# Performance work log

Measured on AMD Instinct MI355X. Metric: run time of the kernel, lower is better.

## Reference

```python
import jax, jax.numpy as jnp
import numpy as np

H = 512   # hidden_size
IN = 5    # input_size
OUT = 2   # output_size
B = 2048
T_HIST = 50


def _lstm_cell(x, h, c, W_ih, W_hh, b_ih, b_hh):
    # PyTorch gate order: i, f, g, o
    z = x @ W_ih.T + h @ W_hh.T + (b_ih + b_hh)
    i, f, g, o = jnp.split(z, 4, axis=-1)
    i = jax.nn.sigmoid(i)
    f = jax.nn.sigmoid(f)
    g = jnp.tanh(g)
    o = jax.nn.sigmoid(o)
    c2 = f * c + i * g
    h2 = o * jnp.tanh(c2)
    return h2, c2


def setup_inputs() -> dict:
    key = jax.random.key(0)
    ks = jax.random.split(key, 20)
    s = 0.05
    inp = {
        "history": jax.random.normal(ks[0], (B, T_HIST, IN), dtype=jnp.float32),
        "future_frames": 30,
        # encoder layer 0 (input IN) and layer 1 (input H)
        "enc_W_ih0": jax.random.normal(ks[1], (4 * H, IN)) * s,
        "enc_W_hh0": jax.random.normal(ks[2], (4 * H, H)) * s,
        "enc_b_ih0": jnp.zeros((4 * H,), jnp.float32),
        "enc_b_hh0": jnp.zeros((4 * H,), jnp.float32),
        "enc_W_ih1": jax.random.normal(ks[3], (4 * H, H)) * s,
        "enc_W_hh1": jax.random.normal(ks[4], (4 * H, H)) * s,
        "enc_b_ih1": jnp.zeros((4 * H,), jnp.float32),
        "enc_b_hh1": jnp.zeros((4 * H,), jnp.float32),
        # decoder layer 0 (input OUT) and layer 1 (input H)
        "dec_W_ih0": jax.random.normal(ks[5], (4 * H, OUT)) * s,
        "dec_W_hh0": jax.random.normal(ks[6], (4 * H, H)) * s,
        "dec_b_ih0": jnp.zeros((4 * H,), jnp.float32),
        "dec_b_hh0": jnp.zeros((4 * H,), jnp.float32),
        "dec_W_ih1": jax.random.normal(ks[7], (4 * H, H)) * s,
        "dec_W_hh1": jax.random.normal(ks[8], (4 * H, H)) * s,
        "dec_b_ih1": jnp.zeros((4 * H,), jnp.float32),
        "dec_b_hh1": jnp.zeros((4 * H,), jnp.float32),
        # output head
        "out_W": jax.random.normal(ks[9], (OUT, H)) * s,
        "out_b": jnp.zeros((OUT,), jnp.float32),
    }
    return inp


def reference(history, enc_W_ih0, enc_W_hh0, enc_b_ih0, enc_b_hh0,
              enc_W_ih1, enc_W_hh1, enc_b_ih1, enc_b_hh1,
              dec_W_ih0, dec_W_hh0, dec_b_ih0, dec_b_hh0,
              dec_W_ih1, dec_W_hh1, dec_b_ih1, dec_b_hh1,
              out_W, out_b, future_frames):
    batch = history.shape[0]
    z = jnp.zeros((batch, H), history.dtype)

    # ----- encoder: 2-layer LSTM over history, scan over time -----
    def enc_step(carry, x_t):
        h0, c0, h1, c1 = carry
        h0, c0 = _lstm_cell(x_t, h0, c0, enc_W_ih0, enc_W_hh0, enc_b_ih0, enc_b_hh0)
        h1, c1 = _lstm_cell(h0, h1, c1, enc_W_ih1, enc_W_hh1, enc_b_ih1, enc_b_hh1)
        return (h0, c0, h1, c1), None

    xs = jnp.swapaxes(history, 0, 1)  # [T, B, IN]
    (h0, c0, h1, c1), _ = jax.lax.scan(enc_step, (z, z, z, z), xs)

    def dec_step(carry, _):
        h0, c0, h1, c1, x_prev = carry
        h0, c0 = _lstm_cell(x_prev, h0, c0, dec_W_ih0, dec_W_hh0, dec_b_ih0, dec_b_hh0)
        h1, c1 = _lstm_cell(h0, h1, c1, dec_W_ih1, dec_W_hh1, dec_b_ih1, dec_b_hh1)
        pred = h1 @ out_W.T + out_b  # [B, OUT]
        return (h0, c0, h1, c1, pred), pred

    x0 = jnp.zeros((batch, OUT), history.dtype)
    _, preds = jax.lax.scan(dec_step, (h0, c0, h1, c1, x0), None, length=future_frames)
    return jnp.swapaxes(preds, 0, 1)  # [B, T_fut, OUT]
```

## Files before the change

### kernel.cpp

```cpp
#include <hip/hip_runtime.h>
#include <hip/hip_bf16.h>


#define HDIM 512
#define BDIM 2048
#define T_HIST 50
#define T_FUT 30

typedef __attribute__((ext_vector_type(8))) short short8;
typedef __attribute__((ext_vector_type(4))) float f32x4;

#define AS1(p) ((const __attribute__((address_space(1))) void*)(p))
#define AS3(p) ((__attribute__((address_space(3))) void*)(p))

__device__ __forceinline__ ushort f2bf(float f) {
    union { float f; unsigned u; } v; v.f = f;
    unsigned r = v.u + 0x7fff + ((v.u >> 16) & 1);
    return (ushort)(r >> 16);
}
__device__ __forceinline__ float bf2f(ushort h) {
    union { unsigned u; float f; } v; v.u = ((unsigned)h) << 16;
    return v.f;
}

__device__ __forceinline__ int swz(int row, int slot) {
    int q = row >> 1;
    int t = ((row & 1) << 2) | slot;
    return q * 8 + (t ^ (q & 7));
}

struct SplitSrc { const float* src[6]; };

__global__ __launch_bounds__(256) void split_weights(SplitSrc s, ushort* __restrict__ hi,
                                                     ushort* __restrict__ lo) {
    int row = blockIdx.x;
    int j = blockIdx.y;
    int g = row >> 9, u = row & 511;
    int rp = (u >> 5) * 128 + ((u >> 4) & 1) * 64 + g * 16 + (u & 15);
    const float* S = s.src[j] + (size_t)row * HDIM;
    ushort* H = hi + ((size_t)j * 2048 + rp) * HDIM;
    ushort* L = lo + ((size_t)j * 2048 + rp) * HDIM;
    for (int k = threadIdx.x; k < HDIM; k += 256) {
        float w = S[k];
        ushort hb = f2bf(w);
        H[k] = hb;
        L[k] = f2bf(w - bf2f(hb));
    }
}

__global__ __launch_bounds__(256) void lstm_cell_mfma(
    const ushort* __restrict__ A1hi, const ushort* __restrict__ A1lo,
    const ushort* __restrict__ W1hi, const ushort* __restrict__ W1lo,
    const ushort* __restrict__ A2hi, const ushort* __restrict__ A2lo,
    const ushort* __restrict__ W2hi, const ushort* __restrict__ W2lo,
    int np,
    const float* __restrict__ x, int x_stride, int Kx, const float* __restrict__ Wx,
    const float* __restrict__ bih, const float* __restrict__ bhh,
    float* __restrict__ c_state, ushort* __restrict__ h_hi, ushort* __restrict__ h_lo)
{
    __shared__ __align__(16) ushort lds[4 * 16384];

    const int tid = threadIdx.x;
    const int w = tid >> 6, l = tid & 63;
    const int wm = w >> 1, wn = w & 1;
    const int lrow = l & 15, lk = l >> 4;

    int id = blockIdx.y * 16 + blockIdx.x;
    int xcd = id & 7, rr = id >> 3;
    int bx = (xcd & 3) * 4 + (rr & 3);
    int by = (xcd >> 2) * 8 + (rr >> 2);
    const int m0 = by * 128;
    const int n0 = bx * 128;
    const int u  = bx * 32 + wn * 16 + lrow;

    f32x4 acc[4][4];

    #pragma unroll
    for (int g = 0; g < 4; ++g) {
        float b = bih[g * HDIM + u] + bhh[g * HDIM + u];
        f32x4 bv = {b, b, b, b};
        #pragma unroll
        for (int fm = 0; fm < 4; ++fm) acc[fm][g] = bv;
    }
    if (Kx > 0) {
        for (int kx = 0; kx < Kx; ++kx) {
            float wv[4];
            #pragma unroll
            for (int g = 0; g < 4; ++g) wv[g] = Wx[(size_t)(g * HDIM + u) * Kx + kx];
            #pragma unroll
            for (int fm = 0; fm < 4; ++fm)
                #pragma unroll
                for (int r = 0; r < 4; ++r) {
                    int m = m0 + wm * 64 + fm * 16 + lk * 4 + r;
                    float xv = x[(size_t)m * x_stride + kx];
                    #pragma unroll
                    for (int g = 0; g < 4; ++g) acc[fm][g][r] += xv * wv[g];
                }
        }
    }

    auto STAGE = [&](int t) {
        int buf = t & 3;
        int p = t >> 4;
        int kc = (t & 15) * 32;
        const ushort* Ah = p ? A2hi : A1hi;
        const ushort* Al = p ? A2lo : A1lo;
        const ushort* Bh = p ? W2hi : W1hi;
        const ushort* Bl = p ? W2lo : W1lo;
        ushort* base = &lds[buf * 16384];
        #pragma unroll
        for (int it = 0; it < 2; ++it) {
            int db = (w * 2 + it) * 64;
            int d = db + l;
            int q = d >> 3, tp = d & 7;
            int tl = tp ^ (q & 7);
            int r = (q << 1) | (tl >> 2);
            int s = tl & 3;
            size_t go = (size_t)r * HDIM + kc + s * 8;
            __builtin_amdgcn_global_load_lds(AS1(Ah + (size_t)m0 * HDIM + go),
                                             AS3(base + db * 8), 16, 0, 0);
            __builtin_amdgcn_global_load_lds(AS1(Al + (size_t)m0 * HDIM + go),
                                             AS3(base + 4096 + db * 8), 16, 0, 0);
            __builtin_amdgcn_global_load_lds(AS1(Bh + (size_t)n0 * HDIM + go),
                                             AS3(base + 8192 + db * 8), 16, 0, 0);
            __builtin_amdgcn_global_load_lds(AS1(Bl + (size_t)n0 * HDIM + go),
                                             AS3(base + 12288 + db * 8), 16, 0, 0);
        }
    };

    const int nch = np * 16;
    STAGE(0);
    STAGE(1);

    for (int t = 0; t < nch; ++t) {
        if (t + 2 < nch) {
            STAGE(t + 2);
            asm volatile("s_waitcnt vmcnt(16)" ::: "memory");
        } else if (t + 1 < nch) {
            asm volatile("s_waitcnt vmcnt(8)" ::: "memory");
        } else {
            asm volatile("s_waitcnt vmcnt(0)" ::: "memory");
        }
        __builtin_amdgcn_s_barrier();
        __builtin_amdgcn_sched_barrier(0);

        ushort* base = &lds[(t & 3) * 16384];
        short8 ah[4], al[4], bh[4], bl[4];
        #pragma unroll
        for (int fm = 0; fm < 4; ++fm) {
            int row = wm * 64 + fm * 16 + lrow;
            int off = swz(row, lk) * 8;
            ah[fm] = *(const short8*)(base + off);
            al[fm] = *(const short8*)(base + 4096 + off);
        }
        #pragma unroll
        for (int g = 0; g < 4; ++g) {
            int row = wn * 64 + g * 16 + lrow;
            int off = swz(row, lk) * 8;
            bh[g] = *(const short8*)(base + 8192 + off);
            bl[g] = *(const short8*)(base + 12288 + off);
        }
        #pragma unroll
        for (int fm = 0; fm < 4; ++fm)
            #pragma unroll
            for (int g = 0; g < 4; ++g)
                acc[fm][g] = __builtin_amdgcn_mfma_f32_16x16x32_bf16(
                    ah[fm], bh[g], acc[fm][g], 0, 0, 0);
        #pragma unroll
        for (int fm = 0; fm < 4; ++fm)
            #pragma unroll
            for (int g = 0; g < 4; ++g)
                acc[fm][g] = __builtin_amdgcn_mfma_f32_16x16x32_bf16(
                    al[fm], bh[g], acc[fm][g], 0, 0, 0);
        #pragma unroll
        for (int fm = 0; fm < 4; ++fm)
            #pragma unroll
            for (int g = 0; g < 4; ++g)
                acc[fm][g] = __builtin_amdgcn_mfma_f32_16x16x32_bf16(
                    ah[fm], bl[g], acc[fm][g], 0, 0, 0);
    }

    #pragma unroll
    for (int fm = 0; fm < 4; ++fm)
        #pragma unroll
        for (int r = 0; r < 4; ++r) {
            int m = m0 + wm * 64 + fm * 16 + lk * 4 + r;
            size_t idx = (size_t)m * HDIM + u;
            float zi = acc[fm][0][r], zf = acc[fm][1][r];
            float zg = acc[fm][2][r], zo = acc[fm][3][r];
            float ig = 1.f / (1.f + __expf(-zi));
            float fg = 1.f / (1.f + __expf(-zf));
            float gg = 2.f / (1.f + __expf(-2.f * zg)) - 1.f;
            float og = 1.f / (1.f + __expf(-zo));
            float cn = fg * c_state[idx] + ig * gg;
            float hn = og * (2.f / (1.f + __expf(-2.f * cn)) - 1.f);
            c_state[idx] = cn;
            ushort hb = f2bf(hn);
            h_hi[idx] = hb;
            h_lo[idx] = f2bf(hn - bf2f(hb));
        }
}

__global__ __launch_bounds__(256) void head_kernel(
    const ushort* __restrict__ hhi, const ushort* __restrict__ hlo,
    const float* __restrict__ Wout, const float* __restrict__ bout,
    float* __restrict__ out, float* __restrict__ xbuf, int t)
{
    int wave = (blockIdx.x * 256 + threadIdx.x) >> 6;
    int lane = threadIdx.x & 63;
    const ushort* hr = hhi + (size_t)wave * HDIM;
    const ushort* lr = hlo + (size_t)wave * HDIM;
    float s0 = 0.f, s1 = 0.f;
    #pragma unroll
    for (int k = lane; k < HDIM; k += 64) {
        float hv = bf2f(hr[k]) + bf2f(lr[k]);
        s0 += hv * Wout[k];
        s1 += hv * Wout[HDIM + k];
    }
    #pragma unroll
    for (int off = 32; off > 0; off >>= 1) {
        s0 += __shfl_down(s0, off);
        s1 += __shfl_down(s1, off);
    }
    if (lane == 0) {
        float p0 = s0 + bout[0], p1 = s1 + bout[1];
        out[(size_t)wave * (T_FUT * 2) + t * 2 + 0] = p0;
        out[(size_t)wave * (T_FUT * 2) + t * 2 + 1] = p1;
        xbuf[wave * 2 + 0] = p0;
        xbuf[wave * 2 + 1] = p1;
    }
}

extern "C" void kernel_launch(void* const* d_in, const int* in_sizes, int n_in,
                              void* d_out, int out_size, void* d_ws, size_t ws_size,
                              hipStream_t stream) {
    const float* history = (const float*)d_in[0];
    const float* eWih0 = (const float*)d_in[2];
    const float* eWhh0 = (const float*)d_in[3];
    const float* ebih0 = (const float*)d_in[4];
    const float* ebhh0 = (const float*)d_in[5];
    const float* eWih1 = (const float*)d_in[6];
    const float* eWhh1 = (const float*)d_in[7];
    const float* ebih1 = (const float*)d_in[8];
    const float* ebhh1 = (const float*)d_in[9];
    const float* dWih0 = (const float*)d_in[10];
    const float* dWhh0 = (const float*)d_in[11];
    const float* dbih0 = (const float*)d_in[12];
    const float* dbhh0 = (const float*)d_in[13];
    const float* dWih1 = (const float*)d_in[14];
    const float* dWhh1 = (const float*)d_in[15];
    const float* dbih1 = (const float*)d_in[16];
    const float* dbhh1 = (const float*)d_in[17];
    const float* outW  = (const float*)d_in[18];
    const float* outb  = (const float*)d_in[19];
    float* out = (float*)d_out;

    const size_t M = (size_t)2048 * 512;
    ushort* whi = (ushort*)d_ws;
    ushort* wlo = whi + 6 * M;
    ushort* hb  = wlo + 6 * M;
    float*  c0  = (float*)(hb + 8 * M);
    float*  c1  = c0 + M;
    float*  xbuf = c1 + M;

    ushort* h0a_hi = hb + 0 * M; ushort* h0a_lo = hb + 1 * M;
    ushort* h0b_hi = hb + 2 * M; ushort* h0b_lo = hb + 3 * M;
    ushort* h1a_hi = hb + 4 * M; ushort* h1a_lo = hb + 5 * M;
    ushort* h1b_hi = hb + 6 * M; ushort* h1b_lo = hb + 7 * M;

    hipMemsetAsync(h0a_hi, 0, 2 * M * sizeof(ushort), stream);
    hipMemsetAsync(h1a_hi, 0, 2 * M * sizeof(ushort), stream);
    hipMemsetAsync(c0, 0, 2 * M * sizeof(float), stream);
    hipMemsetAsync(xbuf, 0, BDIM * 2 * sizeof(float), stream);

    SplitSrc ss;
    ss.src[0] = eWhh0; ss.src[1] = eWih1; ss.src[2] = eWhh1;
    ss.src[3] = dWhh0; ss.src[4] = dWih1; ss.src[5] = dWhh1;
    split_weights<<<dim3(2048, 6), 256, 0, stream>>>(ss, whi, wlo);

    #define WHI(j) (whi + (size_t)(j) * M)
    #define WLO(j) (wlo + (size_t)(j) * M)

    dim3 cgrid(16, 16);
    dim3 blk(256);

    for (int s = 0; s < T_HIST + T_FUT; ++s) {
        ushort* h0r_hi = (s & 1) ? h0b_hi : h0a_hi;
        ushort* h0r_lo = (s & 1) ? h0b_lo : h0a_lo;
        ushort* h0w_hi = (s & 1) ? h0a_hi : h0b_hi;
        ushort* h0w_lo = (s & 1) ? h0a_lo : h0b_lo;
        ushort* h1r_hi = (s & 1) ? h1b_hi : h1a_hi;
        ushort* h1r_lo = (s & 1) ? h1b_lo : h1a_lo;
        ushort* h1w_hi = (s & 1) ? h1a_hi : h1b_hi;
        ushort* h1w_lo = (s & 1) ? h1a_lo : h1b_lo;

        if (s < T_HIST) {
            lstm_cell_mfma<<<cgrid, blk, 0, stream>>>(
                h0r_hi, h0r_lo, WHI(0), WLO(0),
                nullptr, nullptr, nullptr, nullptr, 1,
                history + s * 5, T_HIST * 5, 5, eWih0,
                ebih0, ebhh0, c0, h0w_hi, h0w_lo);
            lstm_cell_mfma<<<cgrid, blk, 0, stream>>>(
                h0w_hi, h0w_lo, WHI(1), WLO(1),
                h1r_hi, h1r_lo, WHI(2), WLO(2), 2,
                nullptr, 0, 0, nullptr,
                ebih1, ebhh1, c1, h1w_hi, h1w_lo);
        } else {
            lstm_cell_mfma<<<cgrid, blk, 0, stream>>>(
                h0r_hi, h0r_lo, WHI(3), WLO(3),
                nullptr, nullptr, nullptr, nullptr, 1,
                xbuf, 2, 2, dWih0,
                dbih0, dbhh0, c0, h0w_hi, h0w_lo);
            lstm_cell_mfma<<<cgrid, blk, 0, stream>>>(
                h0w_hi, h0w_lo, WHI(4), WLO(4),
                h1r_hi, h1r_lo, WHI(5), WLO(5), 2,
                nullptr, 0, 0, nullptr,
                dbih1, dbhh1, c1, h1w_hi, h1w_lo);
            head_kernel<<<512, blk, 0, stream>>>(h1w_hi, h1w_lo, outW, outb,
                                                 out, xbuf, s - T_HIST);
        }
    }
    #undef WHI
    #undef WLO
}
```

Before: 4.140 ms.

## Run encoder layer-1 step alongside next layer-0 step in one launch

Introduces a descriptor-driven `lstm_cells` kernel that runs two independent LSTM cells in a single 512-block grid. During encoding, layer 1 at step s runs together with layer 0 at step s+1, a wavefront schedule that roughly halves the number of encoder launches and fills the GPU with two blocks per CU. To fit two blocks per CU, LDS is cut from four stage buffers to two, and the three-deep prefetch with explicit vmcnt waits becomes a simpler double buffer guarded by `__syncthreads`. The shallower pipeline may expose more memory latency per block. Layer-1 blocks do twice the work of layer-0 blocks, so the fused grid is load-imbalanced.

```diff
diff --git a/kernel.cpp b/kernel.cpp
--- a/kernel.cpp
+++ b/kernel.cpp
@@ -48,24 +48,26 @@
     }
 }
 
-__global__ __launch_bounds__(256) void lstm_cell_mfma(
-    const ushort* __restrict__ A1hi, const ushort* __restrict__ A1lo,
-    const ushort* __restrict__ W1hi, const ushort* __restrict__ W1lo,
-    const ushort* __restrict__ A2hi, const ushort* __restrict__ A2lo,
-    const ushort* __restrict__ W2hi, const ushort* __restrict__ W2lo,
-    int np,
-    const float* __restrict__ x, int x_stride, int Kx, const float* __restrict__ Wx,
-    const float* __restrict__ bih, const float* __restrict__ bhh,
-    float* __restrict__ c_state, ushort* __restrict__ h_hi, ushort* __restrict__ h_lo)
-{
-    __shared__ __align__(16) ushort lds[4 * 16384];
+struct CellDesc {
+    const ushort *A1h, *A1l, *W1h, *W1l;
+    const ushort *A2h, *A2l, *W2h, *W2l;
+    const float *x; const float *Wx;
+    const float *bih, *bhh;
+    float* c; ushort *hh; ushort *hl;
+    int np, xs, Kx;
+};
+
+__global__ __launch_bounds__(256, 2) void lstm_cells(CellDesc dA, CellDesc dB) {
+    __shared__ __align__(16) ushort lds[2 * 16384];
+
+    const CellDesc d = (blockIdx.x >> 8) ? dB : dA;
 
     const int tid = threadIdx.x;
     const int w = tid >> 6, l = tid & 63;
     const int wm = w >> 1, wn = w & 1;
     const int lrow = l & 15, lk = l >> 4;
 
-    int id = blockIdx.y * 16 + blockIdx.x;
+    int id = blockIdx.x & 255;
     int xcd = id & 7, rr = id >> 3;
     int bx = (xcd & 3) * 4 + (rr & 3);
     int by = (xcd >> 2) * 8 + (rr >> 2);
@@ -77,22 +79,22 @@
 
     #pragma unroll
     for (int g = 0; g < 4; ++g) {
-        float b = bih[g * HDIM + u] + bhh[g * HDIM + u];
+        float b = d.bih[g * HDIM + u] + d.bhh[g * HDIM + u];
         f32x4 bv = {b, b, b, b};
         #pragma unroll
         for (int fm = 0; fm < 4; ++fm) acc[fm][g] = bv;
     }
-    if (Kx > 0) {
-        for (int kx = 0; kx < Kx; ++kx) {
+    if (d.Kx > 0) {
+        for (int kx = 0; kx < d.Kx; ++kx) {
             float wv[4];
             #pragma unroll
-            for (int g = 0; g < 4; ++g) wv[g] = Wx[(size_t)(g * HDIM + u) * Kx + kx];
+            for (int g = 0; g < 4; ++g) wv[g] = d.Wx[(size_t)(g * HDIM + u) * d.Kx + kx];
             #pragma unroll
             for (int fm = 0; fm < 4; ++fm)
                 #pragma unroll
                 for (int r = 0; r < 4; ++r) {
                     int m = m0 + wm * 64 + fm * 16 + lk * 4 + r;
-                    float xv = x[(size_t)m * x_stride + kx];
+                    float xv = d.x[(size_t)m * d.xs + kx];
                     #pragma unroll
                     for (int g = 0; g < 4; ++g) acc[fm][g][r] += xv * wv[g];
                 }
@@ -100,19 +102,19 @@
     }
 
     auto STAGE = [&](int t) {
-        int buf = t & 3;
+        int buf = t & 1;
         int p = t >> 4;
         int kc = (t & 15) * 32;
-        const ushort* Ah = p ? A2hi : A1hi;
-        const ushort* Al = p ? A2lo : A1lo;
-        const ushort* Bh = p ? W2hi : W1hi;
-        const ushort* Bl = p ? W2lo : W1lo;
+        const ushort* Ah = p ? d.A2h : d.A1h;
+        const ushort* Al = p ? d.A2l : d.A1l;
+        const ushort* Bh = p ? d.W2h : d.W1h;
+        const ushort* Bl = p ? d.W2l : d.W1l;
         ushort* base = &lds[buf * 16384];
         #pragma unroll
         for (int it = 0; it < 2; ++it) {
             int db = (w * 2 + it) * 64;
-            int d = db + l;
-            int q = d >> 3, tp = d & 7;
+            int dd = db + l;
+            int q = dd >> 3, tp = dd & 7;
             int tl = tp ^ (q & 7);
             int r = (q << 1) | (tl >> 2);
             int s = tl & 3;
@@ -128,23 +130,13 @@
         }
     };
 
-    const int nch = np * 16;
+    const int nch = d.np * 16;
     STAGE(0);
-    STAGE(1);
 
     for (int t = 0; t < nch; ++t) {
-        if (t + 2 < nch) {
-            STAGE(t + 2);
-            asm volatile("s_waitcnt vmcnt(16)" ::: "memory");
-        } else if (t + 1 < nch) {
-            asm volatile("s_waitcnt vmcnt(8)" ::: "memory");
-        } else {
-            asm volatile("s_waitcnt vmcnt(0)" ::: "memory");
-        }
-        __builtin_amdgcn_s_barrier();
-        __builtin_amdgcn_sched_barrier(0);
-
-        ushort* base = &lds[(t & 3) * 16384];
+        __syncthreads();
+        if (t + 1 < nch) STAGE(t + 1);
+        ushort* base = &lds[(t & 1) * 16384];
         short8 ah[4], al[4], bh[4], bl[4];
         #pragma unroll
         for (int fm = 0; fm < 4; ++fm) {
@@ -192,12 +184,12 @@
             float fg = 1.f / (1.f + __expf(-zf));
             float gg = 2.f / (1.f + __expf(-2.f * zg)) - 1.f;
             float og = 1.f / (1.f + __expf(-zo));
-            float cn = fg * c_state[idx] + ig * gg;
+            float cn = fg * d.c[idx] + ig * gg;
             float hn = og * (2.f / (1.f + __expf(-2.f * cn)) - 1.f);
-            c_state[idx] = cn;
+            d.c[idx] = cn;
             ushort hb = f2bf(hn);
-            h_hi[idx] = hb;
-            h_lo[idx] = f2bf(hn - bf2f(hb));
+            d.hh[idx] = hb;
+            d.hl[idx] = f2bf(hn - bf2f(hb));
         }
 }
 
@@ -281,43 +273,65 @@
     #define WHI(j) (whi + (size_t)(j) * M)
     #define WLO(j) (wlo + (size_t)(j) * M)
 
-    dim3 cgrid(16, 16);
+    auto H0R_HI = [&](int s){ return (s & 1) ? h0b_hi : h0a_hi; };
+    auto H0R_LO = [&](int s){ return (s & 1) ? h0b_lo : h0a_lo; };
+    auto H0W_HI = [&](int s){ return (s & 1) ? h0a_hi : h0b_hi; };
+    auto H0W_LO = [&](int s){ return (s & 1) ? h0a_lo : h0b_lo; };
+    auto H1R_HI = [&](int s){ return (s & 1) ? h1b_hi : h1a_hi; };
+    auto H1R_LO = [&](int s){ return (s & 1) ? h1b_lo : h1a_lo; };
+    auto H1W_HI = [&](int s){ return (s & 1) ? h1a_hi : h1b_hi; };
+    auto H1W_LO = [&](int s){ return (s & 1) ? h1a_lo : h1b_lo; };
+
+    auto mkL0enc = [&](int s) {
+        CellDesc d{};
+        d.A1h = H0R_HI(s); d.A1l = H0R_LO(s); d.W1h = WHI(0); d.W1l = WLO(0);
+        d.np = 1; d.x = history + s * 5; d.xs = T_HIST * 5; d.Kx = 5; d.Wx = eWih0;
+        d.bih = ebih0; d.bhh = ebhh0; d.c = c0; d.hh = H0W_HI(s); d.hl = H0W_LO(s);
+        return d;
+    };
+    auto mkL1enc = [&](int s) {
+        CellDesc d{};
+        d.A1h = H0W_HI(s); d.A1l = H0W_LO(s); d.W1h = WHI(1); d.W1l = WLO(1);
+        d.A2h = H1R_HI(s); d.A2l = H1R_LO(s); d.W2h = WHI(2); d.W2l = WLO(2);
+        d.np = 2; d.Kx = 0; d.xs = 0;
+        d.bih = ebih1; d.bhh = ebhh1; d.c = c1; d.hh = H1W_HI(s); d.hl = H1W_LO(s);
+        return d;
+    };
+    auto mkD0 = [&](int s) {
+        CellDesc d{};
+        d.A1h = H0R_HI(s); d.A1l = H0R_LO(s); d.W1h = WHI(3); d.W1l = WLO(3);
+        d.np = 1; d.x = xbuf; d.xs = 2; d.Kx = 2; d.Wx = dWih0;
+        d.bih = dbih0; d.bhh = dbhh0; d.c = c0; d.hh = H0W_HI(s); d.hl = H0W_LO(s);
+        return d;
+    };
+    auto mkD1 = [&](int s) {
+        CellDesc d{};
+        d.A1h = H0W_HI(s); d.A1l = H0W_LO(s); d.W1h = WHI(4); d.W1l = WLO(4);
+        d.A2h = H1R_HI(s); d.A2l = H1R_LO(s); d.W2h = WHI(5); d.W2l = WLO(5);
+        d.np = 2; d.Kx = 0; d.xs = 0;
+        d.bih = dbih1; d.bhh = dbhh1; d.c = c1; d.hh = H1W_HI(s); d.hl = H1W_LO(s);
+        return d;
+    };
+
     dim3 blk(256);
 
-    for (int s = 0; s < T_HIST + T_FUT; ++s) {
-        ushort* h0r_hi = (s & 1) ? h0b_hi : h0a_hi;
-        ushort* h0r_lo = (s & 1) ? h0b_lo : h0a_lo;
-        ushort* h0w_hi = (s & 1) ? h0a_hi : h0b_hi;
-        ushort* h0w_lo = (s & 1) ? h0a_lo : h0b_lo;
-        ushort* h1r_hi = (s & 1) ? h1b_hi : h1a_hi;
-        ushort* h1r_lo = (s & 1) ? h1b_lo : h1a_lo;
-        ushort* h1w_hi = (s & 1) ? h1a_hi : h1b_hi;
-        ushort* h1w_lo = (s & 1) ? h1a_lo : h1b_lo;
-
-        if (s < T_HIST) {
-            lstm_cell_mfma<<<cgrid, blk, 0, stream>>>(
-                h0r_hi, h0r_lo, WHI(0), WLO(0),
-                nullptr, nullptr, nullptr, nullptr, 1,
-                history + s * 5, T_HIST * 5, 5, eWih0,
-                ebih0, ebhh0, c0, h0w_hi, h0w_lo);
-            lstm_cell_mfma<<<cgrid, blk, 0, stream>>>(
-                h0w_hi, h0w_lo, WHI(1), WLO(1),
-                h1r_hi, h1r_lo, WHI(2), WLO(2), 2,
-                nullptr, 0, 0, nullptr,
-                ebih1, ebhh1, c1, h1w_hi, h1w_lo);
-        } else {
-            lstm_cell_mfma<<<cgrid, blk, 0, stream>>>(
-                h0r_hi, h0r_lo, WHI(3), WLO(3),
-                nullptr, nullptr, nullptr, nullptr, 1,
-                xbuf, 2, 2, dWih0,
-                dbih0, dbhh0, c0, h0w_hi, h0w_lo);
-            lstm_cell_mfma<<<cgrid, blk, 0, stream>>>(
-                h0w_hi, h0w_lo, WHI(4), WLO(4),
-                h1r_hi, h1r_lo, WHI(5), WLO(5), 2,
-                nullptr, 0, 0, nullptr,
-                dbih1, dbhh1, c1, h1w_hi, h1w_lo);
-            head_kernel<<<512, blk, 0, stream>>>(h1w_hi, h1w_lo, outW, outb,
-                                                 out, xbuf, s - T_HIST);
+    {
+        CellDesc d = mkL0enc(0);
+        lstm_cells<<<256, blk, 0, stream>>>(d, d);
+    }
+    for (int s = 0; s < T_HIST; ++s) {
+        CellDesc dL1 = mkL1enc(s);
+        CellDesc dNx = (s + 1 < T_HIST) ? mkL0enc(s + 1) : mkD0(T_HIST);
+        lstm_cells<<<512, blk, 0, stream>>>(dL1, dNx);
+    }
+    for (int s = T_HIST; s < T_HIST + T_FUT; ++s) {
+        CellDesc d1 = mkD1(s);
+        lstm_cells<<<256, blk, 0, stream>>>(d1, d1);
+        head_kernel<<<512, blk, 0, stream>>>(H1W_HI(s), H1W_LO(s), outW, outb,
+                                             out, xbuf, s - T_HIST);
+        if (s + 1 < T_HIST + T_FUT) {
+            CellDesc d0 = mkD0(s + 1);
+            lstm_cells<<<256, blk, 0, stream>>>(d0, d0);
         }
     }
     #undef WHI
```

Measured after the change: 3.772 ms (median of 2 runs). -8.9%, faster.
